# Optimization experiments

Hardware: AMD Instinct MI355X
Metric: run time of the kernel (lower is better)

## Reference

```python
import jax, jax.numpy as jnp
import numpy as np

TOP_P = 0.9  # forward default arg, fixed to exercise the top-p path


def setup_inputs() -> dict:
    key = jax.random.key(0)
    k1, k2 = jax.random.split(key)
    B, V = 128, 128000
    logits = jax.random.normal(k1, (B, V), dtype=jnp.float32) * 2.0
    # temperatures in [0.5, 1.5) to avoid divide-by-near-zero
    temperatures = jax.random.uniform(k2, (B,), dtype=jnp.float32, minval=0.5, maxval=1.5)
    return {"logits": logits, "temperatures": temperatures, "top_k": 50}


def reference(logits, temperatures, top_k):
    B, V = logits.shape
    neg_inf = jnp.float32(-jnp.inf)

    # temperature scale + softmax
    scaled = logits.astype(jnp.float32) / temperatures[:, None]
    probs = jax.nn.softmax(scaled, axis=-1)  # (B, V)

    brow = jnp.arange(B)[:, None]

    # top-k filter: keep top-k probs, fill rest with -inf (matches torch scatter into full(-inf))
    if top_k > 0:
        k = min(top_k, V)
        vals, idx = jax.lax.top_k(probs, k)  # (B, k)
        probs = jnp.full_like(probs, neg_inf).at[brow, idx].set(vals)

    # top-p (nucleus) filter: sort desc, cumsum, mask tail beyond top_p (always keep first)
    if TOP_P < 1.0:
        order = jnp.argsort(-probs, axis=-1)              # descending order indices (-inf sorts last)
        sorted_probs = jnp.take_along_axis(probs, order, axis=-1)
        cum = jnp.cumsum(sorted_probs, axis=-1)
        remove = cum > TOP_P
        remove = remove.at[:, 0].set(False)
        sorted_probs = jnp.where(remove, neg_inf, sorted_probs)
        probs = probs.at[brow, order].set(sorted_probs)   # scatter back to original positions

    # Gumbel-max-style sampling: argmax(probs / Exp(1) noise), noise clamped to >= 1e-10
    kn = jax.random.fold_in(jax.random.key(0), 1)
    noise = jnp.maximum(jax.random.exponential(kn, probs.shape, dtype=jnp.float32), 1e-10)
    return jnp.argmax(probs / noise, axis=-1)  # (B,) int tokens
```

## Files before the change

### kernel.cpp

```cpp
#include <hip/hip_runtime.h>
#include <stdint.h>
#include <limits.h>

#define THREEFRY_PARTITIONABLE 1

#define NTK   1024
#define NWAVE (NTK/64)
#define NBUCK 4096
#define BPT   (NBUCK/NTK)
#define CAP   2048
#define KMAX  512

#if __has_builtin(__builtin_amdgcn_exp2f)
#define FAST_EXP2(x) __builtin_amdgcn_exp2f(x)
#else
#define FAST_EXP2(x) exp2f(x)
#endif

__device__ __forceinline__ uint32_t rotl32(uint32_t v, int r) {
  return (v << r) | (v >> (32 - r));
}
__device__ __forceinline__ void tfround(uint32_t& x0, uint32_t& x1, int r) {
  x0 += x1; x1 = rotl32(x1, r); x1 ^= x0;
}
__device__ __forceinline__ void threefry2x32(uint32_t k0, uint32_t k1,
                                             uint32_t x0, uint32_t x1,
                                             uint32_t& o0, uint32_t& o1) {
  uint32_t k2 = k0 ^ k1 ^ 0x1BD11BDAu;
  x0 += k0; x1 += k1;
  tfround(x0,x1,13); tfround(x0,x1,15); tfround(x0,x1,26); tfround(x0,x1,6);
  x0 += k1; x1 += k2 + 1u;
  tfround(x0,x1,17); tfround(x0,x1,29); tfround(x0,x1,16); tfround(x0,x1,24);
  x0 += k2; x1 += k0 + 2u;
  tfround(x0,x1,13); tfround(x0,x1,15); tfround(x0,x1,26); tfround(x0,x1,6);
  x0 += k0; x1 += k1 + 3u;
  tfround(x0,x1,17); tfround(x0,x1,29); tfround(x0,x1,16); tfround(x0,x1,24);
  x0 += k1; x1 += k2 + 4u;
  tfround(x0,x1,13); tfround(x0,x1,15); tfround(x0,x1,26); tfround(x0,x1,6);
  x0 += k2; x1 += k0 + 5u;
  o0 = x0; o1 = x1;
}
__device__ __forceinline__ float jax_noise(uint32_t kn0, uint32_t kn1,
                                           unsigned long long i,
                                           unsigned long long total) {
  uint32_t o0, o1, bits;
#if THREEFRY_PARTITIONABLE
  threefry2x32(kn0, kn1, (uint32_t)(i >> 32), (uint32_t)(i & 0xFFFFFFFFull), o0, o1);
  bits = o0 ^ o1;
#else
  unsigned long long H = total >> 1;
  if (i < H) { threefry2x32(kn0, kn1, (uint32_t)i, (uint32_t)(i + H), o0, o1); bits = o0; }
  else       { threefry2x32(kn0, kn1, (uint32_t)(i - H), (uint32_t)i, o0, o1); bits = o1; }
#endif
  float u = __uint_as_float((bits >> 9) | 0x3f800000u) - 1.0f;
  float e = -log1pf(-u);
  return fmaxf(e, 1e-10f);
}
__device__ __forceinline__ uint32_t fkey(float f) {
  uint32_t u = __float_as_uint(f);
  return u ^ ((u >> 31) ? 0xFFFFFFFFu : 0x80000000u);
}
__device__ __forceinline__ float unfkey_floor(uint32_t keyT) {
  if (keyT == 0u) return -INFINITY;
  return __uint_as_float((keyT & 0x80000000u) ? (keyT ^ 0x80000000u) : ~keyT);
}
__device__ __forceinline__ int clamp_k(int k) {
  if (k < 1) k = 1;
  if (k > KMAX) k = KMAX;
  return k;
}

__device__ __forceinline__ void block_kth_bucket(uint32_t* hist, uint32_t* wtot,
                                                 int* beta_sh, int k,
                                                 int tid, int lane, int wave) {
  const int base = tid * BPT;
  uint32_t tsum = 0;
#pragma unroll
  for (int j = 0; j < BPT; j++) tsum += hist[base + j];
  uint32_t incl = tsum;
  for (int off = 1; off < 64; off <<= 1) {
    uint32_t v = __shfl_down(incl, off);
    if (lane + off < 64) incl += v;
  }
  if (lane == 0) wtot[wave] = incl;
  __syncthreads();
  uint32_t above = incl - tsum;
  for (int w = wave + 1; w < NWAVE; w++) above += wtot[w];
  if (above < (uint32_t)k && above + tsum >= (uint32_t)k) {
    uint32_t run = above;
    for (int j = BPT - 1; j >= 0; j--) {
      run += hist[base + j];
      if (run >= (uint32_t)k) { *beta_sh = base + j; break; }
    }
  }
  __syncthreads();
}

__global__ __launch_bounds__(NTK, 1)
void sampler_fused(const float* __restrict__ logits,
                   const float* __restrict__ temps,
                   const int* __restrict__ topk_ptr,
                   int* __restrict__ out,
                   int B, int V) {
  const int b = blockIdx.x;
  const int tid = threadIdx.x, lane = tid & 63, wave = tid >> 6;

  __shared__ uint32_t hist[NBUCK];
  __shared__ float cv[CAP];
  __shared__ int   ci[CAP];
  __shared__ float cp[CAP];
  __shared__ float sv[KMAX];
  __shared__ int   si[KMAX];
  __shared__ float sc[KMAX];
  __shared__ float wm[NWAVE];
  __shared__ double wsum[NWAVE];
  __shared__ uint32_t wtot[NWAVE];
  __shared__ int beta_sh, cnum_sh, L_sh;
  __shared__ float m_sh, D_sh;

  if (tid == 0) { beta_sh = 0; cnum_sh = 0; }
  for (int i = tid; i < NBUCK; i += NTK) hist[i] = 0;
  __syncthreads();

  const float T = temps[b];
  const float cf = (float)(1.4426950408889634 / (double)T);
  const int k = clamp_k(*topk_ptr);
  const float* row = logits + (size_t)b * (size_t)V;
  const int n4 = ((V & 3) == 0) ? (V >> 2) : 0;
  const float4* row4 = (const float4*)row;

  float v0 = -INFINITY, v1 = -INFINITY, v2 = -INFINITY;
  int   i0 = 0, i1 = 0;
  float a0 = 0.f, a1 = 0.f, a2 = 0.f, a3 = 0.f;

  auto proc = [&](float f, int idx) {
    bool gt0 = f > v0;
    bool gt1 = f > v1;
    bool gt2 = f > v2;
    float nv2 = gt1 ? v1 : (gt2 ? f : v2);
    float nv1 = gt0 ? v0 : (gt1 ? f : v1);
    int   ni1 = gt0 ? i0 : (gt1 ? idx : i1);
    v2 = nv2;
    v1 = nv1; i1 = ni1;
    v0 = gt0 ? f : v0;
    i0 = gt0 ? idx : i0;
  };
  auto proc4 = [&](float4 f, int vb, float& a) {
    proc(f.x, vb); proc(f.y, vb + 1); proc(f.z, vb + 2); proc(f.w, vb + 3);
    a += (FAST_EXP2(f.x * cf) + FAST_EXP2(f.y * cf))
       + (FAST_EXP2(f.z * cf) + FAST_EXP2(f.w * cf));
  };

  int i = tid;
  for (; i + 7 * NTK < n4; i += 8 * NTK) {
    float4 f0 = row4[i];
    float4 f1 = row4[i + NTK];
    float4 f2 = row4[i + 2 * NTK];
    float4 f3 = row4[i + 3 * NTK];
    float4 f4 = row4[i + 4 * NTK];
    float4 f5 = row4[i + 5 * NTK];
    float4 f6 = row4[i + 6 * NTK];
    float4 f7 = row4[i + 7 * NTK];
    proc4(f0, i * 4, a0);
    proc4(f1, (i + NTK) * 4, a1);
    proc4(f2, (i + 2 * NTK) * 4, a2);
    proc4(f3, (i + 3 * NTK) * 4, a3);
    proc4(f4, (i + 4 * NTK) * 4, a0);
    proc4(f5, (i + 5 * NTK) * 4, a1);
    proc4(f6, (i + 6 * NTK) * 4, a2);
    proc4(f7, (i + 7 * NTK) * 4, a3);
  }
  for (; i + 3 * NTK < n4; i += 4 * NTK) {
    float4 fa = row4[i];
    float4 fb = row4[i + NTK];
    float4 fc = row4[i + 2 * NTK];
    float4 fd = row4[i + 3 * NTK];
    proc4(fa, i * 4, a0);
    proc4(fb, (i + NTK) * 4, a1);
    proc4(fc, (i + 2 * NTK) * 4, a2);
    proc4(fd, (i + 3 * NTK) * 4, a3);
  }
  for (; i < n4; i += NTK) {
    float4 fa = row4[i];
    proc4(fa, i * 4, a0);
  }
  for (int v = n4 * 4 + tid; v < V; v += NTK) {
    float f = row[v];
    proc(f, v);
    a0 += FAST_EXP2(f * cf);
  }

  float bm = v0;
  for (int off = 32; off; off >>= 1)
    bm = fmaxf(bm, __shfl_down(bm, off));
  if (lane == 0) wm[wave] = bm;

  double ds = ((double)a0 + (double)a1) + ((double)a2 + (double)a3);
  for (int off = 32; off; off >>= 1)
    ds += __shfl_down(ds, off);
  if (lane == 0) wsum[wave] = ds;

  if (v0 != -INFINITY) atomicAdd(&hist[fkey(v0) >> 20], 1u);
  if (v1 != -INFINITY) atomicAdd(&hist[fkey(v1) >> 20], 1u);
  __syncthreads();

  if (tid == 0) {
    float mg = wm[0];
#pragma unroll
    for (int w = 1; w < NWAVE; w++) mg = fmaxf(mg, wm[w]);
    double t = 0.0;
    for (int w = 0; w < NWAVE; w++) t += wsum[w];
    const double cd = 1.4426950408889634 / (double)T;
    D_sh = (float)(t * exp2(-(double)mg * cd));
    m_sh = mg / T;
  }

  block_kth_bucket(hist, wtot, &beta_sh, k, tid, lane, wave);

  const float fT = unfkey_floor((uint32_t)beta_sh << 20);
  auto emit1 = [&](float f, int idx) {
    if (f >= fT) {
      int p = atomicAdd(&cnum_sh, 1);
      if (p < CAP) { cv[p] = f; ci[p] = idx; }
    }
  };
  auto emit4 = [&](float4 f, int vb) {
    emit1(f.x, vb); emit1(f.y, vb + 1); emit1(f.z, vb + 2); emit1(f.w, vb + 3);
  };
  if (v2 >= fT) {
    int i2 = tid;
    for (; i2 + 3 * NTK < n4; i2 += 4 * NTK) {
      float4 fa = row4[i2];
      float4 fb = row4[i2 + NTK];
      float4 fc = row4[i2 + 2 * NTK];
      float4 fd = row4[i2 + 3 * NTK];
      emit4(fa, i2 * 4);
      emit4(fb, (i2 + NTK) * 4);
      emit4(fc, (i2 + 2 * NTK) * 4);
      emit4(fd, (i2 + 3 * NTK) * 4);
    }
    for (; i2 < n4; i2 += NTK) {
      float4 fa = row4[i2];
      emit4(fa, i2 * 4);
    }
    for (int v = n4 * 4 + tid; v < V; v += NTK) {
      float f = row[v];
      emit1(f, v);
    }
  } else {
    if (v0 >= fT) { int p = atomicAdd(&cnum_sh, 1); if (p < CAP) { cv[p] = v0; ci[p] = i0; } }
    if (v1 >= fT) { int p = atomicAdd(&cnum_sh, 1); if (p < CAP) { cv[p] = v1; ci[p] = i1; } }
  }
  __syncthreads();

  const int C = min(cnum_sh, CAP);
  const float m = m_sh, D = D_sh;
  for (int t = tid; t < C; t += NTK)
    cp[t] = expf(cv[t] / T - m) / D;
  __syncthreads();

  for (int t = tid; t < C; t += NTK) {
    float pi = cp[t];
    int   ii = ci[t];
    int r = 0;
    for (int j = 0; j < C; j++) {
      float pj = cp[j];
      r += (pj > pi) || (pj == pi && ci[j] < ii);
    }
    if (r < k) { sv[r] = pi; si[r] = ii; }
  }
  __syncthreads();

  const int kk = (k < C) ? k : C;

  {
    uint32_t kn0, kn1;
    threefry2x32(0u, 0u, 0u, 1u, kn0, kn1);
    unsigned long long total = (unsigned long long)B * (unsigned long long)V;
    for (int j = tid; j < kk; j += NTK) {
      unsigned long long flat = (unsigned long long)b * (unsigned long long)V
                              + (unsigned long long)si[j];
      sc[j] = sv[j] / jax_noise(kn0, kn1, flat, total);
    }
  }

  if (tid == 0) {
    float cum = 0.f;
    int L = 1;
    bool stop = false;
    for (int j0 = 0; j0 < kk && !stop; j0 += 8) {
      float t0 = sv[j0],     t1 = sv[j0 + 1], t2 = sv[j0 + 2], t3 = sv[j0 + 3];
      float t4 = sv[j0 + 4], t5 = sv[j0 + 5], t6 = sv[j0 + 6], t7 = sv[j0 + 7];
      float tt[8] = {t0, t1, t2, t3, t4, t5, t6, t7};
#pragma unroll
      for (int q = 0; q < 8; q++) {
        int j = j0 + q;
        if (j >= kk) { stop = true; break; }
        cum += tt[q];
        if (j == 0) continue;
        if (cum <= 0.9f) L = j + 1;
        else { stop = true; break; }
      }
    }
    L_sh = L;
  }
  __syncthreads();

  if (wave == 0) {
    const int L = L_sh;
    float bs = -1.0f;
    int   bi = INT_MAX;
    for (int j = lane; j < L; j += 64) {
      float s = sc[j];
      int   ix = si[j];
      if (s > bs || (s == bs && ix < bi)) { bs = s; bi = ix; }
    }
    for (int off = 32; off; off >>= 1) {
      float os = __shfl_down(bs, off);
      int   oi = __shfl_down(bi, off);
      if (os > bs || (os == bs && oi < bi)) { bs = os; bi = oi; }
    }
    if (lane == 0) out[b] = bi;
  }
}

extern "C" void kernel_launch(void* const* d_in, const int* in_sizes, int n_in,
                              void* d_out, int out_size, void* d_ws, size_t ws_size,
                              hipStream_t stream) {
  const float* logits = (const float*)d_in[0];
  const float* temps  = (const float*)d_in[1];
  const int*   topk   = (const int*)d_in[2];
  int* out = (int*)d_out;

  int B = in_sizes[1];
  int V = in_sizes[0] / B;

  sampler_fused<<<dim3(B), dim3(NTK), 0, stream>>>(logits, temps, topk, out, B, V);
}
```

Baseline: 109.9 us.

## Split each row across multiple blocks with a separate finalize kernel

Replaces the one-block-per-row fused sampler with a two-kernel scheme. Each row is split into about eight chunks of roughly 16K elements, and every chunk block computes a partial max, exp-sum, histogram threshold and top candidates into workspace. A finalize kernel then merges the partials and performs the rank sort, noise and top-p selection. The goal is to fill the GPU, since 128 single-block rows underuse the chip's CUs, at the cost of a second launch, workspace traffic, and a per-chunk candidate cap of 256 that could drop candidates.

```diff
diff --git a/kernel.cpp b/kernel.cpp
--- a/kernel.cpp
+++ b/kernel.cpp
@@ -6,10 +6,15 @@
 
 #define NTK   1024
 #define NWAVE (NTK/64)
+#define NTK1  512
+#define NW1   (NTK1/64)
 #define NBUCK 4096
-#define BPT   (NBUCK/NTK)
 #define CAP   2048
+#define CAPS  256
+#define CAPG  2048
 #define KMAX  512
+#define SMAX  32
+#define CHUNK_TARGET 16384
 
 #if __has_builtin(__builtin_amdgcn_exp2f)
 #define FAST_EXP2(x) __builtin_amdgcn_exp2f(x)
@@ -70,13 +75,15 @@
   return k;
 }
 
+template<int NT, int NW>
 __device__ __forceinline__ void block_kth_bucket(uint32_t* hist, uint32_t* wtot,
                                                  int* beta_sh, int k,
                                                  int tid, int lane, int wave) {
-  const int base = tid * BPT;
+  constexpr int BPTc = NBUCK / NT;
+  const int base = tid * BPTc;
   uint32_t tsum = 0;
 #pragma unroll
-  for (int j = 0; j < BPT; j++) tsum += hist[base + j];
+  for (int j = 0; j < BPTc; j++) tsum += hist[base + j];
   uint32_t incl = tsum;
   for (int off = 1; off < 64; off <<= 1) {
     uint32_t v = __shfl_down(incl, off);
@@ -85,15 +92,280 @@
   if (lane == 0) wtot[wave] = incl;
   __syncthreads();
   uint32_t above = incl - tsum;
-  for (int w = wave + 1; w < NWAVE; w++) above += wtot[w];
+  for (int w = wave + 1; w < NW; w++) above += wtot[w];
   if (above < (uint32_t)k && above + tsum >= (uint32_t)k) {
     uint32_t run = above;
-    for (int j = BPT - 1; j >= 0; j--) {
+    for (int j = BPTc - 1; j >= 0; j--) {
       run += hist[base + j];
       if (run >= (uint32_t)k) { *beta_sh = base + j; break; }
     }
   }
   __syncthreads();
+}
+
+__global__ __launch_bounds__(NTK1, 8)
+void sampler_stream(const float* __restrict__ logits,
+                    const float* __restrict__ temps,
+                    const int* __restrict__ topk_ptr,
+                    float* __restrict__ msArr,
+                    double* __restrict__ dsumArr,
+                    int* __restrict__ cntArr,
+                    float2* __restrict__ pairs,
+                    int B, int V, int S, int chunk) {
+  const int blk = blockIdx.x;
+  const int b = blk / S, sp = blk - b * S;
+  const int tid = threadIdx.x, lane = tid & 63, wave = tid >> 6;
+
+  __shared__ uint32_t hist[NBUCK];
+  __shared__ float wm[NW1];
+  __shared__ double wsum[NW1];
+  __shared__ uint32_t wtot[NW1];
+  __shared__ int beta_sh, cnum_sh;
+
+  if (tid == 0) { beta_sh = 0; cnum_sh = 0; }
+  for (int i = tid; i < NBUCK; i += NTK1) hist[i] = 0;
+
+  const float T = temps[b];
+  const float cf = (float)(1.4426950408889634 / (double)T);
+  const int k = clamp_k(*topk_ptr);
+
+  const int start = sp * chunk;
+  const int end = min(start + chunk, V);
+  const float* row = logits + (size_t)b * (size_t)V;
+  const int n = (end > start) ? (end - start) : 0;
+  const int n4 = n >> 2;
+  const float4* row4 = (const float4*)(row + start);
+
+  float v0 = -INFINITY, v1 = -INFINITY, v2 = -INFINITY;
+  int   i0 = 0, i1 = 0;
+  float a0 = 0.f, a1 = 0.f, a2 = 0.f, a3 = 0.f;
+
+  auto proc = [&](float f, int idx) {
+    bool gt0 = f > v0;
+    bool gt1 = f > v1;
+    bool gt2 = f > v2;
+    float nv2 = gt1 ? v1 : (gt2 ? f : v2);
+    float nv1 = gt0 ? v0 : (gt1 ? f : v1);
+    int   ni1 = gt0 ? i0 : (gt1 ? idx : i1);
+    v2 = nv2;
+    v1 = nv1; i1 = ni1;
+    v0 = gt0 ? f : v0;
+    i0 = gt0 ? idx : i0;
+  };
+  auto proc4 = [&](float4 f, int vb, float& a) {
+    proc(f.x, vb); proc(f.y, vb + 1); proc(f.z, vb + 2); proc(f.w, vb + 3);
+    a += (FAST_EXP2(f.x * cf) + FAST_EXP2(f.y * cf))
+       + (FAST_EXP2(f.z * cf) + FAST_EXP2(f.w * cf));
+  };
+
+  if (n4 > 0) {
+    const int G = (n4 + NTK1 - 1) / NTK1;
+    for (int g0 = 0; g0 < G; g0 += 8) {
+      float4 f[8];
+#pragma unroll
+      for (int j = 0; j < 8; j++) {
+        int ii = (g0 + j) * NTK1 + tid;
+        int ic = (ii < n4) ? ii : (n4 - 1);
+        f[j] = row4[ic];
+      }
+#pragma unroll
+      for (int j = 0; j < 8; j++) {
+        int ii = (g0 + j) * NTK1 + tid;
+        float4 ff = f[j];
+        if (ii >= n4) { ff.x = -INFINITY; ff.y = -INFINITY; ff.z = -INFINITY; ff.w = -INFINITY; }
+        float& a = (j & 3) == 0 ? a0 : ((j & 3) == 1 ? a1 : ((j & 3) == 2 ? a2 : a3));
+        proc4(ff, start + ii * 4, a);
+      }
+    }
+  }
+  for (int v = start + n4 * 4 + tid; v < end; v += NTK1) {
+    float f = row[v];
+    proc(f, v);
+    a0 += FAST_EXP2(f * cf);
+  }
+
+  float bm = v0;
+  for (int off = 32; off; off >>= 1)
+    bm = fmaxf(bm, __shfl_down(bm, off));
+  if (lane == 0) wm[wave] = bm;
+
+  double ds = ((double)a0 + (double)a1) + ((double)a2 + (double)a3);
+  for (int off = 32; off; off >>= 1)
+    ds += __shfl_down(ds, off);
+  if (lane == 0) wsum[wave] = ds;
+  __syncthreads();
+
+  if (v0 != -INFINITY) atomicAdd(&hist[fkey(v0) >> 20], 1u);
+  if (v1 != -INFINITY) atomicAdd(&hist[fkey(v1) >> 20], 1u);
+  __syncthreads();
+
+  if (tid == 0) {
+    float m_sp = wm[0];
+#pragma unroll
+    for (int w = 1; w < NW1; w++) m_sp = fmaxf(m_sp, wm[w]);
+    msArr[blk] = m_sp;
+    double t = 0.0;
+    for (int w = 0; w < NW1; w++) t += wsum[w];
+    dsumArr[blk] = t;
+  }
+
+  block_kth_bucket<NTK1, NW1>(hist, wtot, &beta_sh, k, tid, lane, wave);
+
+  const float fT = unfkey_floor((uint32_t)beta_sh << 20);
+  float2* myp = pairs + (size_t)blk * CAPS;
+
+  if (v2 >= fT) {
+    for (int i2 = tid; i2 < n4; i2 += NTK1) {
+      float4 f = row4[i2];
+      const int vb = start + i2 * 4;
+      if (f.x >= fT) { int p = atomicAdd(&cnum_sh, 1); if (p < CAPS) myp[p] = make_float2(f.x, __int_as_float(vb)); }
+      if (f.y >= fT) { int p = atomicAdd(&cnum_sh, 1); if (p < CAPS) myp[p] = make_float2(f.y, __int_as_float(vb + 1)); }
+      if (f.z >= fT) { int p = atomicAdd(&cnum_sh, 1); if (p < CAPS) myp[p] = make_float2(f.z, __int_as_float(vb + 2)); }
+      if (f.w >= fT) { int p = atomicAdd(&cnum_sh, 1); if (p < CAPS) myp[p] = make_float2(f.w, __int_as_float(vb + 3)); }
+    }
+    for (int v = start + n4 * 4 + tid; v < end; v += NTK1) {
+      float f = row[v];
+      if (f >= fT) { int p = atomicAdd(&cnum_sh, 1); if (p < CAPS) myp[p] = make_float2(f, __int_as_float(v)); }
+    }
+  } else {
+    if (v0 >= fT) { int p = atomicAdd(&cnum_sh, 1); if (p < CAPS) myp[p] = make_float2(v0, __int_as_float(i0)); }
+    if (v1 >= fT) { int p = atomicAdd(&cnum_sh, 1); if (p < CAPS) myp[p] = make_float2(v1, __int_as_float(i1)); }
+  }
+  __syncthreads();
+  if (tid == 0) cntArr[blk] = min(cnum_sh, CAPS);
+}
+
+__global__ __launch_bounds__(NTK, 1)
+void sampler_finalize(const float* __restrict__ temps,
+                      const int* __restrict__ topk_ptr,
+                      const float* __restrict__ msArr,
+                      const double* __restrict__ dsumArr,
+                      const int* __restrict__ cntArr,
+                      const float2* __restrict__ pairs,
+                      int* __restrict__ out,
+                      int B, int V, int S) {
+  const int b = blockIdx.x;
+  const int tid = threadIdx.x, lane = tid & 63, wave = tid >> 6;
+
+  __shared__ float cv[CAPG];
+  __shared__ int   ci[CAPG];
+  __shared__ float cp[CAPG];
+  __shared__ float sv[KMAX];
+  __shared__ int   si[KMAX];
+  __shared__ float sc[KMAX];
+  __shared__ int   offL[SMAX + 1];
+  __shared__ int   cnL[SMAX];
+  __shared__ float msL[SMAX];
+  __shared__ double dsL[SMAX];
+  __shared__ int   L_sh;
+  __shared__ float m_sh, D_sh;
+
+  const int k = clamp_k(*topk_ptr);
+  const float T = temps[b];
+
+  if (tid < S) {
+    msL[tid] = msArr[b * S + tid];
+    dsL[tid] = dsumArr[b * S + tid];
+    int c = cntArr[b * S + tid];
+    cnL[tid] = (c < CAPS) ? c : CAPS;
+  }
+  __syncthreads();
+
+  if (tid == 0) {
+    int acc = 0;
+    for (int j = 0; j < S; j++) { offL[j] = acc; acc += cnL[j]; }
+    offL[S] = acc;
+    float mg = msL[0];
+    for (int j = 1; j < S; j++) mg = fmaxf(mg, msL[j]);
+    double t = 0.0;
+    for (int j = 0; j < S; j++) t += dsL[j];
+    const double cd = 1.4426950408889634 / (double)T;
+    D_sh = (float)(t * exp2(-(double)mg * cd));
+    m_sh = mg / T;
+  }
+  __syncthreads();
+
+  const int TC = min(offL[S], CAPG);
+  const float m = m_sh, D = D_sh;
+
+  for (int t = tid; t < TC; t += NTK) {
+    int j = 0;
+#pragma unroll
+    for (int jj = 1; jj <= SMAX; jj++)
+      if (jj <= S) j += (t >= offL[jj]);
+    float2 pr = pairs[(size_t)(b * S + j) * CAPS + (t - offL[j])];
+    cv[t] = pr.x;
+    ci[t] = __float_as_int(pr.y);
+  }
+  __syncthreads();
+
+  for (int t = tid; t < TC; t += NTK)
+    cp[t] = expf(cv[t] / T - m) / D;
+  __syncthreads();
+
+  for (int t = tid; t < TC; t += NTK) {
+    float pi = cp[t];
+    int   ii = ci[t];
+    int r = 0;
+    for (int j = 0; j < TC; j++) {
+      float pj = cp[j];
+      r += (pj > pi) || (pj == pi && ci[j] < ii);
+    }
+    if (r < k) { sv[r] = pi; si[r] = ii; }
+  }
+  __syncthreads();
+
+  const int kk = (k < TC) ? k : TC;
+
+  {
+    uint32_t kn0, kn1;
+    threefry2x32(0u, 0u, 0u, 1u, kn0, kn1);
+    unsigned long long total = (unsigned long long)B * (unsigned long long)V;
+    for (int j = tid; j < kk; j += NTK) {
+      unsigned long long flat = (unsigned long long)b * (unsigned long long)V
+                              + (unsigned long long)si[j];
+      sc[j] = sv[j] / jax_noise(kn0, kn1, flat, total);
+    }
+  }
+
+  if (tid == 0) {
+    float cum = 0.f;
+    int L = 1;
+    bool stop = false;
+    for (int j0 = 0; j0 < kk && !stop; j0 += 8) {
+      float t0 = sv[j0],     t1 = sv[j0 + 1], t2 = sv[j0 + 2], t3 = sv[j0 + 3];
+      float t4 = sv[j0 + 4], t5 = sv[j0 + 5], t6 = sv[j0 + 6], t7 = sv[j0 + 7];
+      float tt[8] = {t0, t1, t2, t3, t4, t5, t6, t7};
+#pragma unroll
+      for (int q = 0; q < 8; q++) {
+        int j = j0 + q;
+        if (j >= kk) { stop = true; break; }
+        cum += tt[q];
+        if (j == 0) continue;
+        if (cum <= 0.9f) L = j + 1;
+        else { stop = true; break; }
+      }
+    }
+    L_sh = L;
+  }
+  __syncthreads();
+
+  if (wave == 0) {
+    const int L = L_sh;
+    float bs = -1.0f;
+    int   bi = INT_MAX;
+    for (int j = lane; j < L; j += 64) {
+      float s = sc[j];
+      int   ix = si[j];
+      if (s > bs || (s == bs && ix < bi)) { bs = s; bi = ix; }
+    }
+    for (int off = 32; off; off >>= 1) {
+      float os = __shfl_down(bs, off);
+      int   oi = __shfl_down(bi, off);
+      if (os > bs || (os == bs && oi < bi)) { bs = os; bi = oi; }
+    }
+    if (lane == 0) out[b] = bi;
+  }
 }
 
 __global__ __launch_bounds__(NTK, 1)
@@ -215,7 +487,7 @@
     m_sh = mg / T;
   }
 
-  block_kth_bucket(hist, wtot, &beta_sh, k, tid, lane, wave);
+  block_kth_bucket<NTK, NWAVE>(hist, wtot, &beta_sh, k, tid, lane, wave);
 
   const float fT = unfkey_floor((uint32_t)beta_sh << 20);
   auto emit1 = [&](float f, int idx) {
@@ -224,29 +496,13 @@
       if (p < CAP) { cv[p] = f; ci[p] = idx; }
     }
   };
-  auto emit4 = [&](float4 f, int vb) {
-    emit1(f.x, vb); emit1(f.y, vb + 1); emit1(f.z, vb + 2); emit1(f.w, vb + 3);
-  };
   if (v2 >= fT) {
-    int i2 = tid;
-    for (; i2 + 3 * NTK < n4; i2 += 4 * NTK) {
-      float4 fa = row4[i2];
-      float4 fb = row4[i2 + NTK];
-      float4 fc = row4[i2 + 2 * NTK];
-      float4 fd = row4[i2 + 3 * NTK];
-      emit4(fa, i2 * 4);
-      emit4(fb, (i2 + NTK) * 4);
-      emit4(fc, (i2 + 2 * NTK) * 4);
-      emit4(fd, (i2 + 3 * NTK) * 4);
-    }
-    for (; i2 < n4; i2 += NTK) {
-      float4 fa = row4[i2];
-      emit4(fa, i2 * 4);
-    }
-    for (int v = n4 * 4 + tid; v < V; v += NTK) {
-      float f = row[v];
-      emit1(f, v);
-    }
+    for (int i2 = tid; i2 < n4; i2 += NTK) {
+      float4 f = row4[i2];
+      const int vb = i2 * 4;
+      emit1(f.x, vb); emit1(f.y, vb + 1); emit1(f.z, vb + 2); emit1(f.w, vb + 3);
+    }
+    for (int v = n4 * 4 + tid; v < V; v += NTK) emit1(row[v], v);
   } else {
     if (v0 >= fT) { int p = atomicAdd(&cnum_sh, 1); if (p < CAP) { cv[p] = v0; ci[p] = i0; } }
     if (v1 >= fT) { int p = atomicAdd(&cnum_sh, 1); if (p < CAP) { cv[p] = v1; ci[p] = i1; } }
@@ -272,7 +528,6 @@
   __syncthreads();
 
   const int kk = (k < C) ? k : C;
-
   {
     uint32_t kn0, kn1;
     threefry2x32(0u, 0u, 0u, 1u, kn0, kn1);
@@ -283,7 +538,6 @@
       sc[j] = sv[j] / jax_noise(kn0, kn1, flat, total);
     }
   }
-
   if (tid == 0) {
     float cum = 0.f;
     int L = 1;
@@ -335,5 +589,31 @@
   int B = in_sizes[1];
   int V = in_sizes[0] / B;
 
-  sampler_fused<<<dim3(B), dim3(NTK), 0, stream>>>(logits, temps, topk, out, B, V);
-}
+  int S = (V + CHUNK_TARGET - 1) / CHUNK_TARGET;
+  if (S > SMAX) S = SMAX;
+  if (S < 1) S = 1;
+  size_t need;
+  for (;;) {
+    need = (size_t)B * S * (sizeof(double) + sizeof(float) + sizeof(int))
+         + (size_t)B * S * CAPS * sizeof(float2);
+    if (need <= ws_size || S <= 2) break;
+    S >>= 1;
+  }
+
+  if (ws_size < need || S < 2) {
+    sampler_fused<<<dim3(B), dim3(NTK), 0, stream>>>(logits, temps, topk, out, B, V);
+    return;
+  }
+
+  int chunk = (((V + S - 1) / S) + 3) & ~3;
+
+  double* dsumArr = (double*)d_ws;
+  float*  msArr   = (float*)(dsumArr + (size_t)B * S);
+  int*    cntArr  = (int*)(msArr + (size_t)B * S);
+  float2* pairs   = (float2*)(cntArr + (size_t)B * S);
+
+  sampler_stream<<<dim3(B * S), dim3(NTK1), 0, stream>>>(
+      logits, temps, topk, msArr, dsumArr, cntArr, pairs, B, V, S, chunk);
+  sampler_finalize<<<dim3(B), dim3(NTK), 0, stream>>>(
+      temps, topk, msArr, dsumArr, cntArr, pairs, out, B, V, S);
+}
```

Result: slower. 136.7 us (+24.4%).
